# Performance work log

Measured on AMD Instinct MI355X. Metric: run time of the kernel, lower is better.

Reference implementation:

```python
import jax, jax.numpy as jnp
import numpy as np

MAX_REL = 64  # max_relative_position
LN_EPS = 1e-5


def _relative_positions(seq_len):
    r = jnp.arange(seq_len)
    rel = jnp.clip(r[None, :] - r[:, None], -MAX_REL, MAX_REL) + MAX_REL
    return rel  # [S, S] int32 in [0, 2*MAX_REL]


def setup_inputs() -> dict:
    key = jax.random.key(0)
    ks = jax.random.split(key, 8)
    B, S, H = 8, 1024, 128
    sd = 1.0 / np.sqrt(H)
    return {
        "x": jax.random.normal(ks[0], (B, S, H), jnp.float32),
        "Wq": jax.random.normal(ks[1], (H, H), jnp.float32) * sd,
        "bq": jnp.zeros((H,), jnp.float32),
        "Wk": jax.random.normal(ks[2], (H, H), jnp.float32) * sd,
        "bk": jnp.zeros((H,), jnp.float32),
        "Wv": jax.random.normal(ks[3], (H, H), jnp.float32) * sd,
        "bv": jnp.zeros((H,), jnp.float32),
        "rel_k": jax.random.normal(ks[4], (2 * MAX_REL + 1, H), jnp.float32),
        "rel_v": jax.random.normal(ks[5], (2 * MAX_REL + 1, H), jnp.float32),
        "Wo": jax.random.normal(ks[6], (H, H), jnp.float32) * sd,
        "bo": jnp.zeros((H,), jnp.float32),
        "gamma": jnp.ones((H,), jnp.float32),
        "beta": jnpp if False else jnp.zeros((H,), jnp.float32),
    }


def reference(x, Wq, bq, Wk, bk, Wv, bv, rel_k, rel_v, Wo, bo, gamma, beta):
    B, S, H = x.shape
    scale = jnp.sqrt(jnp.asarray(H, x.dtype))

    q = x @ Wq + bq  # [B,S,H]
    k = x @ Wk + bk
    v = x @ Wv + bv

    scores = jnp.einsum("bih,bjh->bij", q, k) / scale  # [B,S,S]

    relpos = _relative_positions(S)            # [S,S] int
    rk = rel_k[relpos]                          # [S,S,H] gather
    scores = scores + jnp.einsum("bih,ijh->bij", q, rk)

    attn = jax.nn.softmax(scores, axis=-1)      # dropout = identity (eval)

    ctx = jnp.einsum("bij,bjh->bih", attn, v)
    rv = rel_v[relpos]                          # [S,S,H] gather
    ctx = ctx + jnp.einsum("bij,ijh->bih", attn, rv)

    out = ctx @ Wo + bo

    # residual + LayerNorm
    y = out + x
    mu = jnp.mean(y, axis=-1, keepdims=True)
    var = jnp.mean(jnp.square(y - mu), axis=-1, keepdims=True)
    y = (y - mu) * jax.lax.rsqrt(var + LN_EPS) * gamma + beta
    return y, attn
```

## Files before the change

kernel.cpp:

```cpp
#include <hip/hip_runtime.h>

constexpr int Bn = 8, Sn = 1024, Hn = 128, Rn = 129, RLD = 132;
constexpr float INV_SCALE = 0.088388347648318447f;
constexpr size_t YEL = (size_t)Bn * Sn * Hn;

typedef short bf16x8 __attribute__((ext_vector_type(8)));
typedef short v4s __attribute__((ext_vector_type(4)));
typedef float f32x4 __attribute__((ext_vector_type(4)));
typedef int v4i __attribute__((ext_vector_type(4)));

__device__ __forceinline__ float bf2f(short s) {
    unsigned u = ((unsigned)(unsigned short)s) << 16;
    float f; __builtin_memcpy(&f, &u, 4); return f;
}
__device__ __forceinline__ short f2bf(float f) {
    unsigned u; __builtin_memcpy(&u, &f, 4);
    unsigned r = (u + 0x7fffu + ((u >> 16) & 1u)) >> 16;
    return (short)(r & 0xffffu);
}

__global__ __launch_bounds__(384) void build_tables(
    const float* __restrict__ rel_k, const float* __restrict__ rel_v,
    const float* __restrict__ Wo,
    short* __restrict__ relcat, short* __restrict__ BcatT)
{
    if (blockIdx.x < Rn) {
        const int p = blockIdx.x, c = threadIdx.x;
        const int j = (c < 256) ? (c & 127) : (c - 256);
        float v = rel_k[p * Hn + j];
        short h = f2bf(v);
        relcat[p * 384 + c] = (c < 256) ? h : f2bf(v - bf2f(h));
    } else {
        int idx = (blockIdx.x - Rn) * 384 + threadIdx.x;
        if (idx < 320 * 128) {
            int k = idx >> 7, n = idx & 127;
            float v;
            if (k < 128) v = Wo[k * Hn + n];
            else if (k < 257) {
                int p = k - 128; float a = 0.f;
                for (int h = 0; h < Hn; ++h) a += rel_v[p * Hn + h] * Wo[h * Hn + n];
                v = a;
            } else v = 0.f;
            BcatT[n * 320 + k] = f2bf(v);
        }
    }
}

__global__ __launch_bounds__(256) void proj(
    const float* __restrict__ X,
    const float* __restrict__ Wq, const float* __restrict__ bq,
    const float* __restrict__ Wk, const float* __restrict__ bk,
    const float* __restrict__ Wv, const float* __restrict__ bv,
    short* __restrict__ qh, short* __restrict__ qcat,
    short* __restrict__ kh, short* __restrict__ vT)
{
    __shared__ float xs[64][128];
    __shared__ float wsm[32][128];
    const int tid = threadIdx.x;
    const int sel = blockIdx.y;
    const int row0 = blockIdx.x * 64;
    const float* W = (sel == 0) ? Wq : (sel == 1) ? Wk : Wv;
    const float* bias = (sel == 0) ? bq : (sel == 1) ? bk : bv;

#pragma unroll
    for (int it = 0; it < 8; ++it) {
        int u = tid + it * 256;
        int r = u >> 5, c4 = (u & 31) * 4;
        *(float4*)&xs[r][c4] = *(const float4*)(X + (size_t)(row0 + r) * 128 + c4);
    }

    const int rg = tid >> 5, cg = tid & 31;
    float acc[8][4] = {};
    for (int kc = 0; kc < 128; kc += 32) {
#pragma unroll
        for (int it = 0; it < 4; ++it) {
            int u = tid + it * 256;
            int kk = u >> 5, c4 = (u & 31) * 4;
            *(float4*)&wsm[kk][c4] = *(const float4*)(W + (size_t)(kc + kk) * 128 + c4);
        }
        __syncthreads();
#pragma unroll 8
        for (int kk = 0; kk < 32; ++kk) {
            float wv[4];
#pragma unroll
            for (int c = 0; c < 4; ++c) wv[c] = wsm[kk][cg + c * 32];
#pragma unroll
            for (int r = 0; r < 8; ++r) {
                float xv = xs[rg * 8 + r][kc + kk];
#pragma unroll
                for (int c = 0; c < 4; ++c) acc[r][c] += xv * wv[c];
            }
        }
        __syncthreads();
    }

#pragma unroll
    for (int c = 0; c < 4; ++c) {
        int col = cg + c * 32;
        float bv2 = bias[col];
#pragma unroll
        for (int r = 0; r < 8; ++r) {
            int row = row0 + rg * 8 + r;
            float v = acc[r][c] + bv2;
            short h = f2bf(v);
            if (sel == 0) {
                qh[(size_t)row * 128 + col] = h;
                qcat[(size_t)row * 256 + col] = h;
                qcat[(size_t)row * 256 + 128 + col] = f2bf(v - bf2f(h));
            } else if (sel == 1) {
                kh[(size_t)row * 128 + col] = h;
            } else {
                int b = row >> 10, i = row & (Sn - 1);
                vT[(size_t)b * 131072 + (size_t)col * 1024 + i] = h;
            }
        }
    }
}

__global__ __launch_bounds__(256) void qrel_gemm(
    const short* __restrict__ qcat, const short* __restrict__ relcat,
    float* __restrict__ qrel)
{
    const int tid = threadIdx.x;
    const int wave = tid >> 6, lane = tid & 63;
    const int quad = lane >> 4, l15 = lane & 15;
    const int row0 = blockIdx.x * 64, col0 = blockIdx.y * 64;

    const short* arow = qcat + (size_t)(row0 + wave * 16 + l15) * 256;
    f32x4 acc[4] = {};
#pragma unroll
    for (int kc = 0; kc < 384; kc += 32) {
        int srcc = (kc >= 256) ? kc - 256 : kc;
        bf16x8 af = *(const bf16x8*)(arow + srcc + quad * 8);
#pragma unroll
        for (int nt = 0; nt < 4; ++nt) {
            int brow = col0 + nt * 16 + l15;
            bf16x8 bf = {0, 0, 0, 0, 0, 0, 0, 0};
            if (brow < Rn)
                bf = *(const bf16x8*)(relcat + (size_t)brow * 384 + kc + quad * 8);
            acc[nt] = __builtin_amdgcn_mfma_f32_16x16x32_bf16(af, bf, acc[nt], 0, 0, 0);
        }
    }
    const int rloc0 = wave * 16 + quad * 4;
#pragma unroll
    for (int nt = 0; nt < 4; ++nt) {
        int col = col0 + nt * 16 + l15;
#pragma unroll
        for (int r = 0; r < 4; ++r) {
            if (col < Rn)
                qrel[(size_t)(row0 + rloc0 + r) * RLD + col] = acc[nt][r];
        }
    }
}

__global__ __launch_bounds__(512, 4) void fused_attn(
    const short* __restrict__ qh, const short* __restrict__ kh,
    const short* __restrict__ vT, const float* __restrict__ qrel_g,
    const short* __restrict__ BcatT,
    const float* __restrict__ X, const float* __restrict__ bo,
    const float* __restrict__ gamma, const float* __restrict__ beta,
    float* __restrict__ attn_g, float* __restrict__ y_g)
{
    __shared__ __align__(16) char smem[46080];
    short* Pb   = (short*)smem;
    short* CtxA = (short*)(smem + 33024);
    float* QrL  = (float*)(smem + 33024);
    float* redM = (float*)(smem + 44032);
    float* redS = redM + 128;
    float* redL = redS + 128;
    float* redH = redL + 128;

    const int tid = threadIdx.x;
    const int w = tid >> 6, lane = tid & 63;
    const int quad = lane >> 4, l15 = lane & 15;
    const int lb = blockIdx.x + (blockIdx.z << 6);
    const int bz = lb & 7;
    const int row0 = (lb >> 3) << 4;
    const size_t grow0 = (size_t)bz * Sn + row0;

#pragma unroll
    for (int rr = 0; rr < 2; ++rr) {
        int r = w * 2 + rr;
        const float* src = qrel_g + (grow0 + r) * RLD;
        QrL[r * 132 + lane] = src[lane];
        QrL[r * 132 + 64 + lane] = src[64 + lane];
        if (lane < 4) QrL[r * 132 + 128 + lane] = src[128 + lane];
    }

    bf16x8 afr[4];
#pragma unroll
    for (int kk = 0; kk < 4; ++kk)
        afr[kk] = *(const bf16x8*)(qh + (grow0 + l15) * 128 + kk * 32 + quad * 8);

    const short* khb = kh + (size_t)bz * Sn * 128;
    f32x4 acc[8] = {};
#pragma unroll
    for (int kt = 0; kt < 8; ++kt) {
        const short* kr = khb + (size_t)(kt * 128 + w * 16 + l15) * 128;
#pragma unroll
        for (int kk = 0; kk < 4; ++kk) {
            bf16x8 b = *(const bf16x8*)(kr + kk * 32 + quad * 8);
            acc[kt] = __builtin_amdgcn_mfma_f32_16x16x32_bf16(afr[kk], b, acc[kt], 0, 0, 0);
        }
    }
    __syncthreads();

    float mx[4];
#pragma unroll
    for (int r = 0; r < 4; ++r) {
        int lr = quad * 4 + r, i = row0 + lr;
        float m = -3.4e38f;
#pragma unroll
        for (int kt = 0; kt < 8; ++kt) {
            int col = kt * 128 + w * 16 + l15;
            int d = col - i; d = (d < -64) ? -64 : (d > 64 ? 64 : d);
            float v = acc[kt][r] * INV_SCALE + QrL[lr * 132 + d + 64];
            acc[kt][r] = v;
            m = fmaxf(m, v);
        }
#pragma unroll
        for (int msk = 1; msk < 16; msk <<= 1) m = fmaxf(m, __shfl_xor(m, msk));
        if (l15 == 0) redM[lr * 8 + w] = m;
    }
    __syncthreads();
#pragma unroll
    for (int r = 0; r < 4; ++r) {
        int lr = quad * 4 + r;
        float m = redM[lr * 8];
#pragma unroll
        for (int j = 1; j < 8; ++j) m = fmaxf(m, redM[lr * 8 + j]);
        mx[r] = m;
    }

#pragma unroll
    for (int r = 0; r < 4; ++r) {
        int lr = quad * 4 + r, i = row0 + lr;
        float s = 0.f, lo = 0.f, hi = 0.f;
#pragma unroll
        for (int kt = 0; kt < 8; ++kt) {
            float e = __expf(acc[kt][r] - mx[r]);
            acc[kt][r] = e;
            s += e;
            int col = kt * 128 + w * 16 + l15;
            lo += (col <= i - 64) ? e : 0.f;
            hi += (col >= i + 64) ? e : 0.f;
        }
#pragma unroll
        for (int msk = 1; msk < 16; msk <<= 1) {
            s += __shfl_xor(s, msk);
            lo += __shfl_xor(lo, msk);
            hi += __shfl_xor(hi, msk);
        }
        if (l15 == 0) { redS[lr * 8 + w] = s; redL[lr * 8 + w] = lo; redH[lr * 8 + w] = hi; }
    }
    __syncthreads();

#pragma unroll
    for (int r = 0; r < 4; ++r) {
        int lr = quad * 4 + r;
        float s = 0.f;
#pragma unroll
        for (int j = 0; j < 8; ++j) s += redS[lr * 8 + j];
        float inv = 1.0f / s;
#pragma unroll
        for (int kt = 0; kt < 8; ++kt) {
            int col = kt * 128 + w * 16 + l15;
            Pb[lr * 1032 + col] = f2bf(acc[kt][r] * inv);
        }
    }
    __syncthreads();

    {
        float* ab = attn_g + grow0 * Sn;
#pragma unroll
        for (int it = 0; it < 8; ++it) {
            int u = tid + it * 512;
            int r = u >> 8, c4 = (u & 255) * 4;
            v4s pv = *(const v4s*)&Pb[r * 1032 + c4];
            float4 o;
            o.x = bf2f(pv[0]); o.y = bf2f(pv[1]);
            o.z = bf2f(pv[2]); o.w = bf2f(pv[3]);
            *(float4*)(ab + (size_t)r * Sn + c4) = o;
        }
    }

    const short* vtb = vT + (size_t)bz * 131072 + (size_t)(w * 16 + l15) * 1024;
    f32x4 cacc = {};
#pragma unroll
    for (int kc = 0; kc < 8; ++kc) {
#pragma unroll
        for (int kk = 0; kk < 4; ++kk) {
            bf16x8 a = *(const bf16x8*)&Pb[l15 * 1032 + kc * 128 + kk * 32 + quad * 8];
            bf16x8 b = *(const bf16x8*)(vtb + kc * 128 + kk * 32 + quad * 8);
            cacc = __builtin_amdgcn_mfma_f32_16x16x32_bf16(a, b, cacc, 0, 0, 0);
        }
    }

#pragma unroll
    for (int r = 0; r < 4; ++r)
        CtxA[(quad * 4 + r) * 344 + w * 16 + l15] = f2bf(cacc[r]);
#pragma unroll
    for (int rr = 0; rr < 2; ++rr) {
        int lr = w * 2 + rr, i = row0 + lr;
        float s = 0.f, lo = 0.f, hi = 0.f;
#pragma unroll
        for (int j = 0; j < 8; ++j) {
            s += redS[lr * 8 + j]; lo += redL[lr * 8 + j]; hi += redH[lr * 8 + j];
        }
        float inv = 1.0f / s;
        float v0;
        if (lane == 0) v0 = lo * inv;
        else { int c = i + lane - 64; v0 = (c >= 0 && c < Sn) ? bf2f(Pb[lr * 1032 + c]) : 0.f; }
        CtxA[lr * 344 + 128 + lane] = f2bf(v0);
        int c1 = i + lane;
        CtxA[lr * 344 + 192 + lane] = (c1 < Sn) ? Pb[lr * 1032 + c1] : (short)0;
        CtxA[lr * 344 + 256 + lane] = (lane == 0) ? f2bf(hi * inv) : (short)0;
    }
    __syncthreads();

    f32x4 yacc = {};
    const short* bcb = BcatT + (size_t)(w * 16 + l15) * 320;
#pragma unroll
    for (int ch = 0; ch < 3; ++ch) {
        const int nkk = (ch == 2) ? 2 : 4;
#pragma unroll
        for (int kk = 0; kk < 4; ++kk) {
            if (kk >= nkk) break;
            bf16x8 a = *(const bf16x8*)&CtxA[l15 * 344 + ch * 128 + kk * 32 + quad * 8];
            bf16x8 b = *(const bf16x8*)(bcb + ch * 128 + kk * 32 + quad * 8);
            yacc = __builtin_amdgcn_mfma_f32_16x16x32_bf16(a, b, yacc, 0, 0, 0);
        }
    }

    const int col = w * 16 + l15;
    const float bov = bo[col], gv = gamma[col], bev = beta[col];
    float vv[4];
#pragma unroll
    for (int r = 0; r < 4; ++r) {
        int lr = quad * 4 + r;
        vv[r] = yacc[r] + bov + X[(grow0 + lr) * 128 + col];
    }
#pragma unroll
    for (int r = 0; r < 4; ++r) {
        float s = vv[r];
#pragma unroll
        for (int msk = 1; msk < 16; msk <<= 1) s += __shfl_xor(s, msk);
        if (l15 == 0) redM[(quad * 4 + r) * 8 + w] = s;
    }
    __syncthreads();
    float mu[4];
#pragma unroll
    for (int r = 0; r < 4; ++r) {
        int lr = quad * 4 + r;
        float s = 0.f;
#pragma unroll
        for (int j = 0; j < 8; ++j) s += redM[lr * 8 + j];
        mu[r] = s * (1.f / 128.f);
    }
#pragma unroll
    for (int r = 0; r < 4; ++r) {
        float d = vv[r] - mu[r];
        float s = d * d;
#pragma unroll
        for (int msk = 1; msk < 16; msk <<= 1) s += __shfl_xor(s, msk);
        if (l15 == 0) redS[(quad * 4 + r) * 8 + w] = s;
    }
    __syncthreads();
#pragma unroll
    for (int r = 0; r < 4; ++r) {
        int lr = quad * 4 + r;
        float s = 0.f;
#pragma unroll
        for (int j = 0; j < 8; ++j) s += redS[lr * 8 + j];
        float inv = rsqrtf(s * (1.f / 128.f) + 1e-5f);
        y_g[(grow0 + lr) * 128 + col] = (vv[r] - mu[r]) * inv * gv + bev;
    }
}

extern "C" void kernel_launch(void* const* d_in, const int* in_sizes, int n_in,
                              void* d_out, int out_size, void* d_ws, size_t ws_size,
                              hipStream_t stream) {
    const float* x     = (const float*)d_in[0];
    const float* Wq    = (const float*)d_in[1];
    const float* bq    = (const float*)d_in[2];
    const float* Wk    = (const float*)d_in[3];
    const float* bk    = (const float*)d_in[4];
    const float* Wv    = (const float*)d_in[5];
    const float* bv    = (const float*)d_in[6];
    const float* rel_k = (const float*)d_in[7];
    const float* rel_v = (const float*)d_in[8];
    const float* Wo    = (const float*)d_in[9];
    const float* bo    = (const float*)d_in[10];
    const float* gamma = (const float*)d_in[11];
    const float* beta  = (const float*)d_in[12];

    char* ws = (char*)d_ws;
    short* qh     = (short*)(ws + 0);
    short* kh     = (short*)(ws + 2097152);
    short* vT     = (short*)(ws + 4194304);
    short* qcat   = (short*)(ws + 6291456);
    float* qrel   = (float*)(ws + 10485760);
    short* relcat = (short*)(ws + 14811136);
    short* BcatT  = (short*)(ws + 14910464);

    float* y_out = (float*)d_out;
    float* attn  = (float*)d_out + YEL;

    build_tables<<<dim3(Rn + 107), 384, 0, stream>>>(rel_k, rel_v, Wo, relcat, BcatT);
    proj<<<dim3(128, 3), 256, 0, stream>>>(x, Wq, bq, Wk, bk, Wv, bv, qh, qcat, kh, vT);
    qrel_gemm<<<dim3(128, 3), 256, 0, stream>>>(qcat, relcat, qrel);

    fused_attn<<<dim3(64, 1, Bn), 512, 0, stream>>>(
        qh, kh, vT, qrel, BcatT, x, bo, gamma, beta, attn, y_out);
}
```

Baseline: 172.6 us.

## Stage K and V tiles through LDS with async double buffering; tile qrel GEMM in LDS

The fused attention kernel now streams K and V^T through a double-buffered, XOR-swizzled LDS region using global_load_lds. The next 64-column slice loads while MFMAs consume the current one, replacing direct per-lane global fragment loads. The qrel GEMM also stages its A/B tiles through shared memory. The cost is a much larger LDS footprint (about 77KB vs 45KB) and a barrier per slice, which may reduce occupancy under the 4-blocks-per-CU launch bound.

```diff
diff --git a/kernel.cpp b/kernel.cpp
--- a/kernel.cpp
+++ b/kernel.cpp
@@ -17,6 +17,12 @@
     unsigned u; __builtin_memcpy(&u, &f, 4);
     unsigned r = (u + 0x7fffu + ((u >> 16) & 1u)) >> 16;
     return (short)(r & 0xffffu);
+}
+
+__device__ __forceinline__ void gll16(const short* g, short* l) {
+    __builtin_amdgcn_global_load_lds(
+        (const __attribute__((address_space(1))) void*)g,
+        (__attribute__((address_space(3))) void*)l, 16, 0, 0);
 }
 
 __global__ __launch_bounds__(384) void build_tables(
@@ -121,25 +127,43 @@
     const short* __restrict__ qcat, const short* __restrict__ relcat,
     float* __restrict__ qrel)
 {
+    __shared__ short As[64][72];
+    __shared__ short Bs[64][72];
     const int tid = threadIdx.x;
     const int wave = tid >> 6, lane = tid & 63;
     const int quad = lane >> 4, l15 = lane & 15;
     const int row0 = blockIdx.x * 64, col0 = blockIdx.y * 64;
 
-    const short* arow = qcat + (size_t)(row0 + wave * 16 + l15) * 256;
     f32x4 acc[4] = {};
-#pragma unroll
-    for (int kc = 0; kc < 384; kc += 32) {
-        int srcc = (kc >= 256) ? kc - 256 : kc;
-        bf16x8 af = *(const bf16x8*)(arow + srcc + quad * 8);
-#pragma unroll
-        for (int nt = 0; nt < 4; ++nt) {
-            int brow = col0 + nt * 16 + l15;
-            bf16x8 bf = {0, 0, 0, 0, 0, 0, 0, 0};
-            if (brow < Rn)
-                bf = *(const bf16x8*)(relcat + (size_t)brow * 384 + kc + quad * 8);
-            acc[nt] = __builtin_amdgcn_mfma_f32_16x16x32_bf16(af, bf, acc[nt], 0, 0, 0);
-        }
+    for (int kc = 0; kc < 384; kc += 64) {
+#pragma unroll
+        for (int it = 0; it < 2; ++it) {
+            int u = tid + it * 256;
+            int r = u >> 3, c8 = (u & 7) * 8;
+            int srcc = kc + c8;
+            if (srcc >= 256) srcc -= 256;
+            *(v4i*)&As[r][c8] = *(const v4i*)(qcat + (size_t)(row0 + r) * 256 + srcc);
+        }
+#pragma unroll
+        for (int it = 0; it < 2; ++it) {
+            int u = tid + it * 256;
+            int r = u >> 3, c8 = (u & 7) * 8;
+            v4i val = {0, 0, 0, 0};
+            if (col0 + r < Rn)
+                val = *(const v4i*)(relcat + (size_t)(col0 + r) * 384 + kc + c8);
+            *(v4i*)&Bs[r][c8] = val;
+        }
+        __syncthreads();
+#pragma unroll
+        for (int ks = 0; ks < 64; ks += 32) {
+            bf16x8 af = *(const bf16x8*)&As[wave * 16 + l15][ks + quad * 8];
+#pragma unroll
+            for (int nt = 0; nt < 4; ++nt) {
+                bf16x8 bf = *(const bf16x8*)&Bs[nt * 16 + l15][ks + quad * 8];
+                acc[nt] = __builtin_amdgcn_mfma_f32_16x16x32_bf16(af, bf, acc[nt], 0, 0, 0);
+            }
+        }
+        __syncthreads();
     }
     const int rloc0 = wave * 16 + quad * 4;
 #pragma unroll
@@ -161,11 +185,12 @@
     const float* __restrict__ gamma, const float* __restrict__ beta,
     float* __restrict__ attn_g, float* __restrict__ y_g)
 {
-    __shared__ __align__(16) char smem[46080];
-    short* Pb   = (short*)smem;
-    short* CtxA = (short*)(smem + 33024);
-    float* QrL  = (float*)(smem + 33024);
-    float* redM = (float*)(smem + 44032);
+    __shared__ __align__(16) char smem[78848];
+    short* bufS = (short*)smem;
+    short* Pb   = (short*)(smem + 32768);
+    short* CtxA = (short*)(smem + 65792);
+    float* QrL  = (float*)(smem + 65792);
+    float* redM = (float*)(smem + 76800);
     float* redS = redM + 128;
     float* redL = redS + 128;
     float* redH = redL + 128;
@@ -178,6 +203,9 @@
     const int row0 = (lb >> 3) << 4;
     const size_t grow0 = (size_t)bz * Sn + row0;
 
+    const short* khb  = kh + (size_t)bz * Sn * 128;
+    const short* vtb0 = vT + (size_t)bz * 131072;
+
 #pragma unroll
     for (int rr = 0; rr < 2; ++rr) {
         int r = w * 2 + rr;
@@ -192,18 +220,46 @@
     for (int kk = 0; kk < 4; ++kk)
         afr[kk] = *(const bf16x8*)(qh + (grow0 + l15) * 128 + kk * 32 + quad * 8);
 
-    const short* khb = kh + (size_t)bz * Sn * 128;
+    auto stage_kh = [&](int kt2) {
+        const short* base = khb + (size_t)((kt2 >> 1) * 128) * 128 + (kt2 & 1) * 64;
+        short* dst = bufS + (kt2 & 1) * 8192;
+#pragma unroll
+        for (int it = 0; it < 2; ++it) {
+            int g = tid + it * 512;
+            int r = g >> 3, c = g & 7;
+            gll16(base + r * 128 + ((c ^ (r & 7)) * 8), dst + g * 8);
+        }
+    };
+    auto stage_v = [&](int kc2) {
+        const short* base = vtb0 + (kc2 >> 1) * 128 + (kc2 & 1) * 64;
+        short* dst = bufS + (kc2 & 1) * 8192;
+#pragma unroll
+        for (int it = 0; it < 2; ++it) {
+            int g = tid + it * 512;
+            int r = g >> 3, c = g & 7;
+            gll16(base + r * 1024 + ((c ^ (r & 7)) * 8), dst + g * 8);
+        }
+    };
+
+    stage_kh(0);
+    __syncthreads();
     f32x4 acc[8] = {};
 #pragma unroll
-    for (int kt = 0; kt < 8; ++kt) {
-        const short* kr = khb + (size_t)(kt * 128 + w * 16 + l15) * 128;
-#pragma unroll
-        for (int kk = 0; kk < 4; ++kk) {
-            bf16x8 b = *(const bf16x8*)(kr + kk * 32 + quad * 8);
-            acc[kt] = __builtin_amdgcn_mfma_f32_16x16x32_bf16(afr[kk], b, acc[kt], 0, 0, 0);
-        }
-    }
-    __syncthreads();
+    for (int kt2 = 0; kt2 < 16; ++kt2) {
+        if (kt2 < 15) stage_kh(kt2 + 1);
+        const short* hb = bufS + (kt2 & 1) * 8192;
+        const int rb = w * 16 + l15;
+#pragma unroll
+        for (int kk = 0; kk < 2; ++kk) {
+            int j = (kk * 4 + quad) ^ (l15 & 7);
+            bf16x8 b = *(const bf16x8*)(hb + rb * 64 + j * 8);
+            acc[kt2 >> 1] = __builtin_amdgcn_mfma_f32_16x16x32_bf16(
+                afr[(kt2 & 1) * 2 + kk], b, acc[kt2 >> 1], 0, 0, 0);
+        }
+        __syncthreads();
+    }
+
+    stage_v(0);
 
     float mx[4];
 #pragma unroll
@@ -284,16 +340,20 @@
         }
     }
 
-    const short* vtb = vT + (size_t)bz * 131072 + (size_t)(w * 16 + l15) * 1024;
     f32x4 cacc = {};
 #pragma unroll
-    for (int kc = 0; kc < 8; ++kc) {
-#pragma unroll
-        for (int kk = 0; kk < 4; ++kk) {
-            bf16x8 a = *(const bf16x8*)&Pb[l15 * 1032 + kc * 128 + kk * 32 + quad * 8];
-            bf16x8 b = *(const bf16x8*)(vtb + kc * 128 + kk * 32 + quad * 8);
+    for (int kc2 = 0; kc2 < 16; ++kc2) {
+        if (kc2 < 15) stage_v(kc2 + 1);
+        const short* hb = bufS + (kc2 & 1) * 8192;
+        const int rb = w * 16 + l15;
+#pragma unroll
+        for (int kk = 0; kk < 2; ++kk) {
+            bf16x8 a = *(const bf16x8*)&Pb[l15 * 1032 + kc2 * 64 + kk * 32 + quad * 8];
+            int j = (kk * 4 + quad) ^ (l15 & 7);
+            bf16x8 b = *(const bf16x8*)(hb + rb * 64 + j * 8);
             cacc = __builtin_amdgcn_mfma_f32_16x16x32_bf16(a, b, cacc, 0, 0, 0);
         }
+        __syncthreads();
     }
 
 #pragma unroll
```

Result: faster. 158.4 us (-8.2%).

## Stage qrel GEMM tiles in LDS and double-buffer K/V loads in attention

Applied to the files above, without the earlier changes.

The small qrel GEMM now loads 64x64 tiles of qcat and relcat into shared memory cooperatively, instead of each wave reading its B fragments straight from global memory. In the fused attention kernel, the QK^T and PV loops use explicit register double-buffering, so the next K or V fragments are fetched while the current MFMAs run. The fully unrolled loops probably already let the compiler hoist these loads, so the software prefetch may add register pressure under the 512-thread, 4-block launch bounds. The LDS tiling adds barriers to a kernel that is likely small relative to the fused attention kernel.

```diff
diff --git a/kernel.cpp b/kernel.cpp
--- a/kernel.cpp
+++ b/kernel.cpp
@@ -121,25 +121,43 @@
     const short* __restrict__ qcat, const short* __restrict__ relcat,
     float* __restrict__ qrel)
 {
+    __shared__ short As[64][72];
+    __shared__ short Bs[64][72];
     const int tid = threadIdx.x;
     const int wave = tid >> 6, lane = tid & 63;
     const int quad = lane >> 4, l15 = lane & 15;
     const int row0 = blockIdx.x * 64, col0 = blockIdx.y * 64;
 
-    const short* arow = qcat + (size_t)(row0 + wave * 16 + l15) * 256;
     f32x4 acc[4] = {};
-#pragma unroll
-    for (int kc = 0; kc < 384; kc += 32) {
-        int srcc = (kc >= 256) ? kc - 256 : kc;
-        bf16x8 af = *(const bf16x8*)(arow + srcc + quad * 8);
-#pragma unroll
-        for (int nt = 0; nt < 4; ++nt) {
-            int brow = col0 + nt * 16 + l15;
-            bf16x8 bf = {0, 0, 0, 0, 0, 0, 0, 0};
-            if (brow < Rn)
-                bf = *(const bf16x8*)(relcat + (size_t)brow * 384 + kc + quad * 8);
-            acc[nt] = __builtin_amdgcn_mfma_f32_16x16x32_bf16(af, bf, acc[nt], 0, 0, 0);
-        }
+    for (int kc = 0; kc < 384; kc += 64) {
+#pragma unroll
+        for (int it = 0; it < 2; ++it) {
+            int u = tid + it * 256;
+            int r = u >> 3, c8 = (u & 7) * 8;
+            int srcc = kc + c8;
+            if (srcc >= 256) srcc -= 256;
+            *(v4i*)&As[r][c8] = *(const v4i*)(qcat + (size_t)(row0 + r) * 256 + srcc);
+        }
+#pragma unroll
+        for (int it = 0; it < 2; ++it) {
+            int u = tid + it * 256;
+            int r = u >> 3, c8 = (u & 7) * 8;
+            v4i val = {0, 0, 0, 0};
+            if (col0 + r < Rn)
+                val = *(const v4i*)(relcat + (size_t)(col0 + r) * 384 + kc + c8);
+            *(v4i*)&Bs[r][c8] = val;
+        }
+        __syncthreads();
+#pragma unroll
+        for (int ks = 0; ks < 64; ks += 32) {
+            bf16x8 af = *(const bf16x8*)&As[wave * 16 + l15][ks + quad * 8];
+#pragma unroll
+            for (int nt = 0; nt < 4; ++nt) {
+                bf16x8 bf = *(const bf16x8*)&Bs[nt * 16 + l15][ks + quad * 8];
+                acc[nt] = __builtin_amdgcn_mfma_f32_16x16x32_bf16(af, bf, acc[nt], 0, 0, 0);
+            }
+        }
+        __syncthreads();
     }
     const int rloc0 = wave * 16 + quad * 4;
 #pragma unroll
@@ -178,6 +196,9 @@
     const int row0 = (lb >> 3) << 4;
     const size_t grow0 = (size_t)bz * Sn + row0;
 
+    const short* khb  = kh + (size_t)bz * Sn * 128;
+    const short* vtb0 = vT + (size_t)bz * 131072;
+
 #pragma unroll
     for (int rr = 0; rr < 2; ++rr) {
         int r = w * 2 + rr;
@@ -192,15 +213,27 @@
     for (int kk = 0; kk < 4; ++kk)
         afr[kk] = *(const bf16x8*)(qh + (grow0 + l15) * 128 + kk * 32 + quad * 8);
 
-    const short* khb = kh + (size_t)bz * Sn * 128;
+    const short* krow = khb + (size_t)(w * 16 + l15) * 128 + quad * 8;
     f32x4 acc[8] = {};
-#pragma unroll
-    for (int kt = 0; kt < 8; ++kt) {
-        const short* kr = khb + (size_t)(kt * 128 + w * 16 + l15) * 128;
-#pragma unroll
-        for (int kk = 0; kk < 4; ++kk) {
-            bf16x8 b = *(const bf16x8*)(kr + kk * 32 + quad * 8);
-            acc[kt] = __builtin_amdgcn_mfma_f32_16x16x32_bf16(afr[kk], b, acc[kt], 0, 0, 0);
+    {
+        bf16x8 bcur[4], bnxt[4];
+#pragma unroll
+        for (int kk = 0; kk < 4; ++kk)
+            bcur[kk] = *(const bf16x8*)(krow + kk * 32);
+#pragma unroll
+        for (int kt = 0; kt < 8; ++kt) {
+            if (kt < 7) {
+#pragma unroll
+                for (int kk = 0; kk < 4; ++kk)
+                    bnxt[kk] = *(const bf16x8*)(krow + (size_t)(kt + 1) * 128 * 128 + kk * 32);
+            }
+#pragma unroll
+            for (int kk = 0; kk < 4; ++kk)
+                acc[kt] = __builtin_amdgcn_mfma_f32_16x16x32_bf16(afr[kk], bcur[kk], acc[kt], 0, 0, 0);
+            if (kt < 7) {
+#pragma unroll
+                for (int kk = 0; kk < 4; ++kk) bcur[kk] = bnxt[kk];
+            }
         }
     }
     __syncthreads();
@@ -284,15 +317,29 @@
         }
     }
 
-    const short* vtb = vT + (size_t)bz * 131072 + (size_t)(w * 16 + l15) * 1024;
+    const short* vrow = vtb0 + (size_t)(w * 16 + l15) * 1024 + quad * 8;
     f32x4 cacc = {};
-#pragma unroll
-    for (int kc = 0; kc < 8; ++kc) {
-#pragma unroll
-        for (int kk = 0; kk < 4; ++kk) {
-            bf16x8 a = *(const bf16x8*)&Pb[l15 * 1032 + kc * 128 + kk * 32 + quad * 8];
-            bf16x8 b = *(const bf16x8*)(vtb + kc * 128 + kk * 32 + quad * 8);
-            cacc = __builtin_amdgcn_mfma_f32_16x16x32_bf16(a, b, cacc, 0, 0, 0);
+    {
+        bf16x8 bcur[4], bnxt[4];
+#pragma unroll
+        for (int kk = 0; kk < 4; ++kk)
+            bcur[kk] = *(const bf16x8*)(vrow + kk * 32);
+#pragma unroll
+        for (int kc = 0; kc < 8; ++kc) {
+            if (kc < 7) {
+#pragma unroll
+                for (int kk = 0; kk < 4; ++kk)
+                    bnxt[kk] = *(const bf16x8*)(vrow + (kc + 1) * 128 + kk * 32);
+            }
+#pragma unroll
+            for (int kk = 0; kk < 4; ++kk) {
+                bf16x8 a = *(const bf16x8*)&Pb[l15 * 1032 + kc * 128 + kk * 32 + quad * 8];
+                cacc = __builtin_amdgcn_mfma_f32_16x16x32_bf16(a, bcur[kk], cacc, 0, 0, 0);
+            }
+            if (kc < 7) {
+#pragma unroll
+                for (int kk = 0; kk < 4; ++kk) bcur[kk] = bnxt[kk];
+            }
         }
     }
 
```

Result: faster. 168.0 us (-2.7%).
